# Optimization experiments

Hardware: AMD Instinct MI355X
Metric: run time of the kernel (lower is better)

The kernel has to match this reference:

```python
import jax, jax.numpy as jnp
import numpy as np

B, L, D = 1, 2048, 512
NL, N, K = 4, 16, 4
DI = 2 * D          # mamba expand=2
R = D // 16         # dt_rank = ceil(D/16)
H = 4 * D           # mlp hidden


def _ln(x, w, b, eps=1e-5):
    mu = x.mean(-1, keepdims=True)
    v = ((x - mu) ** 2).mean(-1, keepdims=True)
    return (x - mu) * jax.lax.rsqrt(v + eps) * w + b


def _rms(x, w, eps=1e-5):
    return x * jax.lax.rsqrt((x * x).mean(-1, keepdims=True) + eps) * w


def _ssm_scan(delta, Bm, Cm, u, A, Dp):
    # delta,u: (B,L,DI); Bm,Cm: (B,L,N); A: (DI,N); Dp: (DI,)
    def step(h, inp):
        d_t, b_t, c_t, u_t = inp                              # (B,DI),(B,N),(B,N),(B,DI)
        dA = jnp.exp(d_t[..., None] * A)                      # (B,DI,N)
        h = dA * h + (d_t * u_t)[..., None] * b_t[:, None, :]
        y = jnp.einsum('bdn,bn->bd', h, c_t)
        return h, y
    h0 = jnp.zeros((delta.shape[0], DI, N), delta.dtype)
    xs = (delta.swapaxes(0, 1), Bm.swapaxes(0, 1), Cm.swapaxes(0, 1), u.swapaxes(0, 1))
    _, ys = jax.lax.scan(step, h0, xs)
    return ys.swapaxes(0, 1) + u * Dp


def _mamba(h, in_w, cw, cb, xw, dtw, dtb, A_log, Dp, ow):
    xz = h @ in_w.T                                           # (B,L,2*DI)
    x, z = jnp.split(xz, 2, axis=-1)
    # causal depthwise conv1d, kernel K, left pad K-1
    xp = jnp.pad(x, ((0, 0), (K - 1, 0), (0, 0)))
    Ls = x.shape[1]
    x = sum(cw[:, k] * xp[:, k:k + Ls, :] for k in range(K)) + cb
    x = jax.nn.silu(x)
    dbc = x @ xw.T                                            # (B,L,R+2N)
    dt, Bm, Cm = dbc[..., :R], dbc[..., R:R + N], dbc[..., R + N:]
    delta = jax.nn.softplus(dt @ dtw.T + dtb)                 # (B,L,DI)
    A = -jnp.exp(A_log)                                       # (DI,N)
    y = _ssm_scan(delta, Bm, Cm, x, A, Dp)
    y = y * jax.nn.silu(z)
    return y @ ow.T


def _forward(hidden_states, ln1_w, ln1_b, in_proj_w, conv_w, conv_b, x_proj_w,
             dt_proj_w, dt_proj_b, A_log, D_param, out_proj_w, block_norm_w,
             norm_f_w, ln2_w, ln2_b, fc1_w, fc1_b, fc2_w, fc2_b):
    shortcut = hidden_states
    h = _ln(hidden_states, ln1_w, ln1_b)
    residual = None
    for i in range(in_proj_w.shape[0]):
        residual = h if residual is None else h + residual    # residual_in_fp32
        hn = _rms(residual, block_norm_w[i])                  # fused_add_norm prenorm
        h = _mamba(hn, in_proj_w[i], conv_w[i], conv_b[i], x_proj_w[i],
                   dt_proj_w[i], dt_proj_b[i], A_log[i], D_param[i], out_proj_w[i])
    h = _rms(h + residual, norm_f_w)                          # final rms_norm_fn
    h = shortcut + h
    x = _ln(h, ln2_w, ln2_b)
    x = jax.nn.gelu(x @ fc1_w.T + fc1_b)
    x = x @ fc2_w.T + fc2_b
    return h + x


def setup_inputs() -> dict:
    key = jax.random.key(0)
    ks = jax.random.split(key, 9)
    s = 0.02
    return {
        'hidden_states': jax.random.normal(ks[0], (B, L, D), jnp.float32),
        'ln1_w': jnp.ones((D,), jnp.float32),
        'ln1_b': jnp.zeros((D,), jnp.float32),
        'in_proj_w': jax.random.normal(ks[1], (NL, 2 * DI, D), jnp.float32) * s,
        'conv_w': jax.random.normal(ks[2], (NL, DI, K), jnp.float32) * 0.3,
        'conv_b': jnp.zeros((NL, DI), jnp.float32),
        'x_proj_w': jax.random.normal(ks[3], (NL, R + 2 * N, DI), jnp.float32) * s,
        'dt_proj_w': jax.random.normal(ks[4], (NL, DI, R), jnp.float32) * s,
        'dt_proj_b': jax.random.uniform(ks[5], (NL, DI), jnp.float32, -4.0, -2.0),
        'A_log': jnp.tile(jnp.log(jnp.arange(1, N + 1, dtype=jnp.float32)), (NL, DI, 1)),
        'D_param': jnp.ones((NL, DI), jnp.float32),
        'out_proj_w': jax.random.normal(ks[6], (NL, D, DI), jnp.float32) * s,
        'block_norm_w': jnp.ones((NL, D), jnp.float32),
        'norm_f_w': jnp.ones((D,), jnp.float32),
        'ln2_w': jnp.ones((D,), jnp.float32),
        'ln2_b': jnp.zeros((D,), jnp.float32),
        'fc1_w': jax.random.normal(ks[7], (H, D), jnp.float32) * s,
        'fc1_b': jnp.zeros((H,), jnp.float32),
        'fc2_w': jax.random.normal(ks[8], (D, H), jnp.float32) * s,
        'fc2_b': jnp.zeros((D,), jnp.float32),
    }


def reference(hidden_states, ln1_w, ln1_b, in_proj_w, conv_w, conv_b, x_proj_w,
              dt_proj_w, dt_proj_b, A_log, D_param, out_proj_w, block_norm_w,
              norm_f_w, ln2_w, ln2_b, fc1_w, fc1_b, fc2_w, fc2_b):
    return _forward(hidden_states, ln1_w, ln1_b, in_proj_w, conv_w, conv_b,
                    x_proj_w, dt_proj_w, dt_proj_b, A_log, D_param, out_proj_w,
                    block_norm_w, norm_f_w, ln2_w, ln2_b, fc1_w, fc1_b, fc2_w, fc2_b)
```

## Files before the change

kernel.cpp:

```cpp
#include <hip/hip_runtime.h>
#include <hip/hip_bf16.h>
#include <math.h>

#define L_SEQ 2048
#define Dm    512
#define DI    1024
#define Nst   16
#define Kc    4
#define Rr    32
#define NL    4
#define CH    128
#define LC    (L_SEQ / CH)

typedef __attribute__((ext_vector_type(8))) short bf16x8;
typedef __attribute__((ext_vector_type(4))) float f32x4;

__device__ __forceinline__ float act_softplus(float x) {
    return fmaxf(x, 0.f) + log1pf(__expf(-fabsf(x)));
}
__device__ __forceinline__ float act_gelu(float x) {
    float c = 0.7978845608028654f * (x + 0.044715f * x * x * x);
    float t = 1.f - 2.f / (__expf(2.f * c) + 1.f);
    return 0.5f * x * (1.f + t);
}
__device__ __forceinline__ float silu_(float x) {
    return x / (1.f + __expf(-x));
}
__device__ __forceinline__ ushort f2bf(float f) {
    union { float f; unsigned u; } c; c.f = f;
    unsigned r = c.u + 0x7fffu + ((c.u >> 16) & 1u);
    return (ushort)(r >> 16);
}
__device__ __forceinline__ float bf2f(ushort u) {
    union { unsigned u; float f; } c; c.u = ((unsigned)u) << 16;
    return c.f;
}
__device__ __forceinline__ float wave_sum(float v) {
    #pragma unroll
    for (int off = 32; off; off >>= 1) v += __shfl_xor(v, off);
    return v;
}

__global__ __launch_bounds__(256) void cast_all_kernel(
    const float* __restrict__ s0, ushort* __restrict__ d0, int n0,
    const float* __restrict__ s1, ushort* __restrict__ d1, int n1,
    const float* __restrict__ s2, ushort* __restrict__ d2, int n2,
    const float* __restrict__ s3, ushort* __restrict__ d3, int n3,
    const float* __restrict__ s4, ushort* __restrict__ d4, int n4_,
    const float* __restrict__ s5, ushort* __restrict__ d5, int n5)
{
    int i = blockIdx.x * 256 + threadIdx.x;
    const float* s; ushort* d;
    if (i < n0) { s = s0; d = d0; }
    else { i -= n0; if (i < n1) { s = s1; d = d1; }
    else { i -= n1; if (i < n2) { s = s2; d = d2; }
    else { i -= n2; if (i < n3) { s = s3; d = d3; }
    else { i -= n3; if (i < n4_) { s = s4; d = d4; }
    else { i -= n4_; if (i < n5) { s = s5; d = d5; } else return; } } } } }
    float4 v = ((const float4*)s)[i];
    ushort4 o;
    o.x = f2bf(v.x); o.y = f2bf(v.y); o.z = f2bf(v.z); o.w = f2bf(v.w);
    ((ushort4*)d)[i] = o;
}

__global__ __launch_bounds__(256) void ln_rms_kernel(const float* __restrict__ x,
    const float* __restrict__ w, const float* __restrict__ b,
    const float* __restrict__ rw, float* __restrict__ res,
    ushort* __restrict__ hn_bf)
{
    int lane = threadIdx.x & 63, wv = threadIdx.x >> 6;
    int row = blockIdx.x * 4 + wv;
    size_t base = (size_t)row * Dm + lane * 8;
    float v[8];
    *(float4*)(v)     = *(const float4*)(x + base);
    *(float4*)(v + 4) = *(const float4*)(x + base + 4);
    float s = 0.f, ss = 0.f;
    #pragma unroll
    for (int q = 0; q < 8; ++q) { s += v[q]; ss += v[q] * v[q]; }
    s = wave_sum(s); ss = wave_sum(ss);
    float mu = s * (1.f / Dm);
    float rs = rsqrtf(ss * (1.f / Dm) - mu * mu + 1e-5f);
    float wv8[8], bv8[8], rv8[8];
    *(float4*)(wv8)     = *(const float4*)(w + lane * 8);
    *(float4*)(wv8 + 4) = *(const float4*)(w + lane * 8 + 4);
    *(float4*)(bv8)     = *(const float4*)(b + lane * 8);
    *(float4*)(bv8 + 4) = *(const float4*)(b + lane * 8 + 4);
    *(float4*)(rv8)     = *(const float4*)(rw + lane * 8);
    *(float4*)(rv8 + 4) = *(const float4*)(rw + lane * 8 + 4);
    float o[8], ss2 = 0.f;
    #pragma unroll
    for (int q = 0; q < 8; ++q) {
        o[q] = (v[q] - mu) * rs * wv8[q] + bv8[q];
        ss2 += o[q] * o[q];
    }
    *(float4*)(res + base)     = *(float4*)(o);
    *(float4*)(res + base + 4) = *(float4*)(o + 4);
    ss2 = wave_sum(ss2);
    float rr = rsqrtf(ss2 * (1.f / Dm) + 1e-5f);
    bf16x8 hb;
    #pragma unroll
    for (int q = 0; q < 8; ++q) hb[q] = (short)f2bf(o[q] * rr * rv8[q]);
    *(bf16x8*)(hn_bf + base) = hb;
}

__global__ __launch_bounds__(256) void add_rms_kernel(const ushort* __restrict__ hb,
    float* __restrict__ res, const float* __restrict__ w, ushort* __restrict__ rms_out)
{
    int lane = threadIdx.x & 63, wv = threadIdx.x >> 6;
    int row = blockIdx.x * 4 + wv;
    size_t base = (size_t)row * Dm + lane * 8;
    bf16x8 hv = *(const bf16x8*)(hb + base);
    float v[8];
    *(float4*)(v)     = *(const float4*)(res + base);
    *(float4*)(v + 4) = *(const float4*)(res + base + 4);
    float ss = 0.f;
    #pragma unroll
    for (int q = 0; q < 8; ++q) {
        v[q] += bf2f((ushort)hv[q]);
        ss += v[q] * v[q];
    }
    *(float4*)(res + base)     = *(float4*)(v);
    *(float4*)(res + base + 4) = *(float4*)(v + 4);
    ss = wave_sum(ss);
    float rr = rsqrtf(ss * (1.f / Dm) + 1e-5f);
    float wv8[8];
    *(float4*)(wv8)     = *(const float4*)(w + lane * 8);
    *(float4*)(wv8 + 4) = *(const float4*)(w + lane * 8 + 4);
    bf16x8 ob;
    #pragma unroll
    for (int q = 0; q < 8; ++q) ob[q] = (short)f2bf(v[q] * rr * wv8[q]);
    *(bf16x8*)(rms_out + base) = ob;
}

__global__ __launch_bounds__(256) void final_ln2_kernel(const ushort* __restrict__ hb,
    const float* __restrict__ res, const float* __restrict__ shortcut,
    const float* __restrict__ wf, const float* __restrict__ w2,
    const float* __restrict__ b2, float* __restrict__ hout,
    ushort* __restrict__ yb16)
{
    int lane = threadIdx.x & 63, wv = threadIdx.x >> 6;
    int row = blockIdx.x * 4 + wv;
    size_t base = (size_t)row * Dm + lane * 8;
    bf16x8 hv = *(const bf16x8*)(hb + base);
    float v[8];
    *(float4*)(v)     = *(const float4*)(res + base);
    *(float4*)(v + 4) = *(const float4*)(res + base + 4);
    float ss = 0.f;
    #pragma unroll
    for (int q = 0; q < 8; ++q) {
        v[q] += bf2f((ushort)hv[q]);
        ss += v[q] * v[q];
    }
    ss = wave_sum(ss);
    float rs = rsqrtf(ss * (1.f / Dm) + 1e-5f);
    float sc[8], wf8[8];
    *(float4*)(sc)     = *(const float4*)(shortcut + base);
    *(float4*)(sc + 4) = *(const float4*)(shortcut + base + 4);
    *(float4*)(wf8)     = *(const float4*)(wf + lane * 8);
    *(float4*)(wf8 + 4) = *(const float4*)(wf + lane * 8 + 4);
    float t[8], s2 = 0.f, ss2 = 0.f;
    #pragma unroll
    for (int q = 0; q < 8; ++q) {
        t[q] = sc[q] + v[q] * rs * wf8[q];
        s2 += t[q]; ss2 += t[q] * t[q];
    }
    *(float4*)(hout + base)     = *(float4*)(t);
    *(float4*)(hout + base + 4) = *(float4*)(t + 4);
    s2 = wave_sum(s2); ss2 = wave_sum(ss2);
    float mu = s2 * (1.f / Dm);
    float rsig = rsqrtf(ss2 * (1.f / Dm) - mu * mu + 1e-5f);
    float w28[8], b28[8];
    *(float4*)(w28)     = *(const float4*)(w2 + lane * 8);
    *(float4*)(w28 + 4) = *(const float4*)(w2 + lane * 8 + 4);
    *(float4*)(b28)     = *(const float4*)(b2 + lane * 8);
    *(float4*)(b28 + 4) = *(const float4*)(b2 + lane * 8 + 4);
    bf16x8 ob;
    #pragma unroll
    for (int q = 0; q < 8; ++q) ob[q] = (short)f2bf((t[q] - mu) * rsig * w28[q] + b28[q]);
    *(bf16x8*)(yb16 + base) = ob;
}

template<int BM, int BN, int BK, int EPI, int KS = 1>
__global__ __launch_bounds__(256) void gemm_mfma(
    const ushort* __restrict__ A, int lda,
    const ushort* __restrict__ W, int K,
    void* __restrict__ Cout, int ldc,
    const float* __restrict__ bias, const float* __restrict__ addsrc,
    size_t split_stride)
{
    constexpr int ROWB  = BK * 2;
    constexpr int SMASK = (ROWB / 16) - 1;
    constexpr int KK    = BK / 32;
    constexpr int WM = BM / 2, WN = BN / 2;
    constexpr int FM = WM / 16, FN = WN / 16;
    constexpr int ISS_A = (BM * ROWB) / 4096;
    constexpr int ISS_W = (BN * ROWB) / 4096;

    __shared__ __align__(16) ushort As[BM * BK];
    __shared__ __align__(16) ushort Ws[BN * BK];

    int tid = threadIdx.x;
    int wave = tid >> 6, lane = tid & 63;
    int wr = wave >> 1, wc = wave & 1;
    int l16 = lane & 15, lk = lane >> 4;
    int bm = blockIdx.y * BM, bn = blockIdx.x * BN;

    int kbeg = 0, kend = K;
    float* coutf = (float*)Cout;
    if constexpr (KS > 1) {
        int Kper = K / KS;
        kbeg = blockIdx.z * Kper; kend = kbeg + Kper;
        coutf += split_stride * blockIdx.z;
    }

    const ushort* srcA[ISS_A];
    const ushort* srcW[ISS_W];
    #pragma unroll
    for (int s = 0; s < ISS_A; ++s) {
        int off = s * 4096 + wave * 1024 + lane * 16;
        int row = off / ROWB;
        int slot = (off % ROWB) >> 4;
        int col = ((slot ^ (row & SMASK)) << 3);
        srcA[s] = A + (size_t)(bm + row) * lda + col;
    }
    #pragma unroll
    for (int s = 0; s < ISS_W; ++s) {
        int off = s * 4096 + wave * 1024 + lane * 16;
        int row = off / ROWB;
        int slot = (off % ROWB) >> 4;
        int col = ((slot ^ (row & SMASK)) << 3);
        srcW[s] = W + (size_t)(bn + row) * K + col;
    }
    int aoff[FM][KK], woff[FN][KK];
    #pragma unroll
    for (int i = 0; i < FM; ++i) {
        int row = wr * WM + i * 16 + l16;
        #pragma unroll
        for (int kk = 0; kk < KK; ++kk)
            aoff[i][kk] = row * BK + ((((kk << 2) | lk) ^ (row & SMASK)) << 3);
    }
    #pragma unroll
    for (int j = 0; j < FN; ++j) {
        int row = wc * WN + j * 16 + l16;
        #pragma unroll
        for (int kk = 0; kk < KK; ++kk)
            woff[j][kk] = row * BK + ((((kk << 2) | lk) ^ (row & SMASK)) << 3);
    }

    f32x4 acc[FM][FN] = {};

    for (int k0 = kbeg; k0 < kend; k0 += BK) {
        #pragma unroll
        for (int s = 0; s < ISS_A; ++s)
            __builtin_amdgcn_global_load_lds(
                (const __attribute__((address_space(1))) void*)(srcA[s] + k0),
                (__attribute__((address_space(3))) void*)((char*)As + s * 4096 + wave * 1024),
                16, 0, 0);
        #pragma unroll
        for (int s = 0; s < ISS_W; ++s)
            __builtin_amdgcn_global_load_lds(
                (const __attribute__((address_space(1))) void*)(srcW[s] + k0),
                (__attribute__((address_space(3))) void*)((char*)Ws + s * 4096 + wave * 1024),
                16, 0, 0);
        __syncthreads();
        #pragma unroll
        for (int kk = 0; kk < KK; ++kk) {
            bf16x8 af[FM], wf[FN];
            #pragma unroll
            for (int i = 0; i < FM; ++i) af[i] = *(const bf16x8*)(As + aoff[i][kk]);
            #pragma unroll
            for (int j = 0; j < FN; ++j) wf[j] = *(const bf16x8*)(Ws + woff[j][kk]);
            #pragma unroll
            for (int i = 0; i < FM; ++i)
                #pragma unroll
                for (int j = 0; j < FN; ++j)
                    acc[i][j] = __builtin_amdgcn_mfma_f32_16x16x32_bf16(af[i], wf[j], acc[i][j], 0, 0, 0);
        }
        __syncthreads();
    }

    int orow0 = bm + wr * WM, ocol0 = bn + wc * WN;
    #pragma unroll
    for (int j = 0; j < FN; ++j) {
        int col = ocol0 + j * 16 + l16;
        float bj = 0.f;
        if constexpr (EPI == 2 || EPI == 4) bj = bias[col];
        #pragma unroll
        for (int i = 0; i < FM; ++i) {
            #pragma unroll
            for (int r = 0; r < 4; ++r) {
                int row = orow0 + i * 16 + lk * 4 + r;
                float v = acc[i][j][r];
                if constexpr (EPI == 0) {
                    coutf[(size_t)row * ldc + col] = v;
                } else if constexpr (EPI == 1) {
                    ((ushort*)Cout)[(size_t)row * ldc + col] = f2bf(v);
                } else if constexpr (EPI == 2) {
                    ((ushort*)Cout)[(size_t)row * ldc + col] = f2bf(act_gelu(v + bj));
                } else if constexpr (EPI == 4) {
                    ((float*)Cout)[(size_t)row * ldc + col] = v + bj + addsrc[(size_t)row * ldc + col];
                }
            }
        }
    }
}

__global__ __launch_bounds__(256) void xfin_kernel(
    const float* __restrict__ part, const ushort* __restrict__ wdt,
    const float* __restrict__ dtb, float* __restrict__ dbc,
    ushort* __restrict__ delta_bf)
{
    __shared__ float sdt[8][32];
    int tid = threadIdx.x;
    int t0 = blockIdx.x * 8;
    const int S = L_SEQ * 64;
    #pragma unroll
    for (int i = tid; i < 512; i += 256) {
        int tt = i >> 6, c = i & 63;
        int idx = (t0 + tt) * 64 + c;
        float s = part[idx] + part[idx + S] + part[idx + 2 * S] + part[idx + 3 * S];
        if (c < 32) sdt[tt][c] = s;
        else dbc[idx] = s;
    }
    __syncthreads();
    int d0 = tid * 4;
    bf16x8 w[4][4];
    float b4[4];
    #pragma unroll
    for (int q = 0; q < 4; ++q) {
        b4[q] = dtb[d0 + q];
        #pragma unroll
        for (int p = 0; p < 4; ++p)
            w[q][p] = *(const bf16x8*)(wdt + (size_t)(d0 + q) * 32 + p * 8);
    }
    for (int tt = 0; tt < 8; ++tt) {
        float acc[4] = { b4[0], b4[1], b4[2], b4[3] };
        #pragma unroll
        for (int p = 0; p < 4; ++p)
            #pragma unroll
            for (int e = 0; e < 8; ++e) {
                float sv = sdt[tt][p * 8 + e];
                #pragma unroll
                for (int q = 0; q < 4; ++q)
                    acc[q] = fmaf(sv, bf2f((ushort)w[q][p][e]), acc[q]);
            }
        ushort4 o;
        o.x = f2bf(act_softplus(acc[0]));
        o.y = f2bf(act_softplus(acc[1]));
        o.z = f2bf(act_softplus(acc[2]));
        o.w = f2bf(act_softplus(acc[3]));
        *(ushort4*)(delta_bf + (size_t)(t0 + tt) * DI + d0) = o;
    }
}

__global__ __launch_bounds__(256) void conv_silu_kernel(const ushort* __restrict__ xz,
    const float* __restrict__ cw, const float* __restrict__ cb, ushort* __restrict__ xc)
{
    int g = blockIdx.x * 256 + threadIdx.x;
    int e = g * 8;
    int d0 = e & (DI - 1);
    int t = e >> 10;
    float acc[8];
    #pragma unroll
    for (int q = 0; q < 8; ++q) acc[q] = cb[d0 + q];
    float4 cwv[8];
    #pragma unroll
    for (int q = 0; q < 8; ++q) cwv[q] = *(const float4*)(cw + (size_t)(d0 + q) * 4);
    #pragma unroll
    for (int k = 0; k < 4; ++k) {
        int tt = t + k - 3;
        if (tt >= 0) {
            bf16x8 xv = *(const bf16x8*)(xz + (size_t)tt * (2 * DI) + d0);
            #pragma unroll
            for (int q = 0; q < 8; ++q) {
                float wk = (k == 0) ? cwv[q].x : (k == 1) ? cwv[q].y : (k == 2) ? cwv[q].z : cwv[q].w;
                acc[q] = fmaf(wk, bf2f((ushort)xv[q]), acc[q]);
            }
        }
    }
    bf16x8 o;
    #pragma unroll
    for (int q = 0; q < 8; ++q) o[q] = (short)f2bf(silu_(acc[q]));
    *(bf16x8*)(xc + e) = o;
}

__global__ __launch_bounds__(256) void scan_chunk_kernel(
    const ushort* __restrict__ delta, const ushort* __restrict__ u,
    const float* __restrict__ dbc, const float* __restrict__ A_log,
    float* __restrict__ hend, float* __restrict__ aprod)
{
    __shared__ float bs[LC][16];
    int tid = threadIdx.x;
    int c = blockIdx.x;
    int d = blockIdx.y * 256 + tid;
    int t0 = c * LC;
    {
        int tt = tid >> 4, nn = tid & 15;
        bs[tt][nn] = dbc[(size_t)(t0 + tt) * 64 + 32 + nn];
    }
    float A2[16];
    {
        float a[16];
        #pragma unroll
        for (int q = 0; q < 4; ++q)
            *(float4*)(a + q * 4) = ((const float4*)(A_log + (size_t)d * 16))[q];
        #pragma unroll
        for (int n = 0; n < 16; ++n)
            A2[n] = -__expf(a[n]) * 1.44269504f;
    }
    float h[16], ap[16];
    #pragma unroll
    for (int n = 0; n < 16; ++n) { h[n] = 0.f; ap[n] = 1.f; }
    __syncthreads();
    for (int tt = 0; tt < LC; ++tt) {
        int t = t0 + tt;
        float dt_ = bf2f(delta[(size_t)t * DI + d]);
        float du = dt_ * bf2f(u[(size_t)t * DI + d]);
        #pragma unroll
        for (int n = 0; n < 16; ++n) {
            float dA = exp2f(dt_ * A2[n]);
            h[n] = fmaf(dA, h[n], du * bs[tt][n]);
            ap[n] *= dA;
        }
    }
    size_t base = ((size_t)c * DI + d) * 16;
    #pragma unroll
    for (int q = 0; q < 4; ++q) {
        ((float4*)(hend + base))[q]  = *(float4*)(h + q * 4);
        ((float4*)(aprod + base))[q] = *(float4*)(ap + q * 4);
    }
}

__global__ __launch_bounds__(64) void chunk_prefix_kernel(
    const float* __restrict__ hend, float* __restrict__ aprod_hin)
{
    int j = blockIdx.x * 64 + threadIdx.x;
    float h = 0.f;
    for (int cg = 0; cg < CH; cg += 8) {
        float ap[8], he[8];
        #pragma unroll
        for (int q = 0; q < 8; ++q) {
            size_t o = (size_t)(cg + q) * (DI * Nst) + j;
            ap[q] = aprod_hin[o]; he[q] = hend[o];
        }
        #pragma unroll
        for (int q = 0; q < 8; ++q) {
            size_t o = (size_t)(cg + q) * (DI * Nst) + j;
            aprod_hin[o] = h;
            h = fmaf(ap[q], h, he[q]);
        }
    }
}

__global__ __launch_bounds__(256) void scan_apply_kernel(
    const ushort* __restrict__ delta, const ushort* __restrict__ u,
    const float* __restrict__ dbc, const float* __restrict__ A_log,
    const float* __restrict__ Dp, const ushort* __restrict__ xz,
    const float* __restrict__ hin, ushort* __restrict__ y)
{
    __shared__ float bs[LC][16], cs[LC][16];
    int tid = threadIdx.x;
    int c = blockIdx.x;
    int d = blockIdx.y * 256 + tid;
    int t0 = c * LC;
    #pragma unroll
    for (int i = tid; i < LC * 32; i += 256) {
        int tt = i >> 5, k = i & 31;
        float v = dbc[(size_t)(t0 + tt) * 64 + 32 + k];
        if (k < 16) bs[tt][k] = v; else cs[tt][k - 16] = v;
    }
    float A2[16];
    {
        float a[16];
        #pragma unroll
        for (int q = 0; q < 4; ++q)
            *(float4*)(a + q * 4) = ((const float4*)(A_log + (size_t)d * 16))[q];
        #pragma unroll
        for (int n = 0; n < 16; ++n)
            A2[n] = -__expf(a[n]) * 1.44269504f;
    }
    float h[16];
    size_t base = ((size_t)c * DI + d) * 16;
    #pragma unroll
    for (int q = 0; q < 4; ++q)
        *(float4*)(h + q * 4) = ((const float4*)(hin + base))[q];
    float Dval = Dp[d];
    __syncthreads();
    for (int tt = 0; tt < LC; ++tt) {
        int t = t0 + tt;
        float dt_ = bf2f(delta[(size_t)t * DI + d]);
        float u_  = bf2f(u[(size_t)t * DI + d]);
        float du  = dt_ * u_;
        float acc = 0.f;
        #pragma unroll
        for (int n = 0; n < 16; ++n) {
            float dA = exp2f(dt_ * A2[n]);
            h[n] = fmaf(dA, h[n], du * bs[tt][n]);
            acc = fmaf(h[n], cs[tt][n], acc);
        }
        float z = bf2f(xz[(size_t)t * (2 * DI) + DI + d]);
        y[(size_t)t * DI + d] = f2bf((acc + u_ * Dval) * silu_(z));
    }
}

extern "C" void kernel_launch(void* const* d_in, const int* in_sizes, int n_in,
                              void* d_out, int out_size, void* d_ws, size_t ws_size,
                              hipStream_t stream)
{
    const float* hidden     = (const float*)d_in[0];
    const float* ln1_w      = (const float*)d_in[1];
    const float* ln1_b      = (const float*)d_in[2];
    const float* in_proj_w  = (const float*)d_in[3];
    const float* conv_w     = (const float*)d_in[4];
    const float* conv_b     = (const float*)d_in[5];
    const float* x_proj_w   = (const float*)d_in[6];
    const float* dt_proj_w  = (const float*)d_in[7];
    const float* dt_proj_b  = (const float*)d_in[8];
    const float* A_log      = (const float*)d_in[9];
    const float* D_param    = (const float*)d_in[10];
    const float* out_proj_w = (const float*)d_in[11];
    const float* block_norm_w = (const float*)d_in[12];
    const float* norm_f_w   = (const float*)d_in[13];
    const float* ln2_w      = (const float*)d_in[14];
    const float* ln2_b      = (const float*)d_in[15];
    const float* fc1_w      = (const float*)d_in[16];
    const float* fc1_b      = (const float*)d_in[17];
    const float* fc2_w      = (const float*)d_in[18];
    const float* fc2_b      = (const float*)d_in[19];

    char* P = (char*)d_ws;
    auto alloc = [&](size_t bytes) { char* r = P; P += (bytes + 255) & ~(size_t)255; return r; };
    float* hout   = (float*)alloc((size_t)L_SEQ * Dm * 4);
    float* res    = (float*)alloc((size_t)L_SEQ * Dm * 4);
    float* dbc    = (float*)alloc((size_t)L_SEQ * 64 * 4);
    float* part   = (float*)alloc((size_t)4 * L_SEQ * 64 * 4);
    float* hend   = (float*)alloc((size_t)CH * DI * Nst * 4);
    float* aprod  = (float*)alloc((size_t)CH * DI * Nst * 4);
    ushort* h_bf  = (ushort*)alloc((size_t)L_SEQ * Dm * 2);
    ushort* delta_bf = (ushort*)alloc((size_t)L_SEQ * DI * 2);
    ushort* hn_bf = (ushort*)alloc((size_t)L_SEQ * Dm * 2);
    ushort* xz_bf = (ushort*)alloc((size_t)L_SEQ * 2 * DI * 2);
    ushort* xc_bf = (ushort*)alloc((size_t)L_SEQ * DI * 2);
    ushort* yb_bf = (ushort*)alloc((size_t)L_SEQ * DI * 2);
    ushort* w_in  = (ushort*)alloc((size_t)NL * 2 * DI * Dm * 2);
    ushort* w_out = (ushort*)alloc((size_t)NL * Dm * DI * 2);
    ushort* w_x   = (ushort*)alloc((size_t)NL * 64 * DI * 2);
    ushort* w_dt  = (ushort*)alloc((size_t)NL * DI * Rr * 2);
    ushort* w_fc1 = (ushort*)alloc((size_t)(4 * Dm) * Dm * 2);
    ushort* w_fc2 = (ushort*)alloc((size_t)Dm * (4 * Dm) * 2);
    float* out  = (float*)d_out;

    {
        int n0 = NL * 2 * DI * Dm / 4, n1 = NL * Dm * DI / 4, n2 = NL * 64 * DI / 4;
        int n3 = NL * DI * Rr / 4, n4_ = 4 * Dm * Dm / 4, n5 = Dm * 4 * Dm / 4;
        int tot = n0 + n1 + n2 + n3 + n4_ + n5;
        cast_all_kernel<<<(tot + 255) / 256, 256, 0, stream>>>(
            in_proj_w, w_in, n0, out_proj_w, w_out, n1, x_proj_w, w_x, n2,
            dt_proj_w, w_dt, n3, fc1_w, w_fc1, n4_, fc2_w, w_fc2, n5);
    }

    ln_rms_kernel<<<L_SEQ / 4, 256, 0, stream>>>(hidden, ln1_w, ln1_b,
                                                 block_norm_w, res, hn_bf);

    dim3 gscan(CH, DI / 256);
    for (int i = 0; i < NL; ++i) {
        if (i) add_rms_kernel<<<L_SEQ / 4, 256, 0, stream>>>(h_bf, res,
                                                  block_norm_w + i * Dm, hn_bf);
        gemm_mfma<128, 128, 128, 1><<<dim3(2 * DI / 128, L_SEQ / 128), 256, 0, stream>>>(
            hn_bf, Dm, w_in + (size_t)i * 2 * DI * Dm, Dm, xz_bf, 2 * DI, nullptr, nullptr, 0);
        conv_silu_kernel<<<(L_SEQ * DI / 8) / 256, 256, 0, stream>>>(
            xz_bf, conv_w + i * DI * Kc, conv_b + i * DI, xc_bf);
        gemm_mfma<64, 64, 64, 0, 4><<<dim3(1, L_SEQ / 64, 4), 256, 0, stream>>>(
            xc_bf, DI, w_x + (size_t)i * 64 * DI, DI, part, 64, nullptr, nullptr,
            (size_t)L_SEQ * 64);
        xfin_kernel<<<L_SEQ / 8, 256, 0, stream>>>(part, w_dt + (size_t)i * DI * Rr,
                                        dt_proj_b + i * DI, dbc, delta_bf);
        scan_chunk_kernel<<<gscan, 256, 0, stream>>>(delta_bf, xc_bf, dbc,
                                        A_log + (size_t)i * DI * Nst, hend, aprod);
        chunk_prefix_kernel<<<(DI * Nst) / 64, 64, 0, stream>>>(hend, aprod);
        scan_apply_kernel<<<gscan, 256, 0, stream>>>(delta_bf, xc_bf, dbc,
                                        A_log + (size_t)i * DI * Nst,
                                        D_param + i * DI, xz_bf, aprod, yb_bf);
        gemm_mfma<64, 64, 128, 1><<<dim3(Dm / 64, L_SEQ / 64), 256, 0, stream>>>(
            yb_bf, DI, w_out + (size_t)i * Dm * DI, DI, h_bf, Dm, nullptr, nullptr, 0);
    }

    final_ln2_kernel<<<L_SEQ / 4, 256, 0, stream>>>(h_bf, res, hidden, norm_f_w,
                                                ln2_w, ln2_b, hout, hn_bf);
    gemm_mfma<128, 128, 128, 2><<<dim3(2048 / 128, L_SEQ / 128), 256, 0, stream>>>(
        hn_bf, Dm, w_fc1, Dm, xz_bf, 2048, fc1_b, nullptr, 0);
    gemm_mfma<64, 64, 128, 4><<<dim3(Dm / 64, L_SEQ / 64), 256, 0, stream>>>(
        xz_bf, 2048, w_fc2, 2048, out, Dm, fc2_b, hout, 0);
}
```

Baseline: 445.4 us.

## Fuse conv+silu into x_proj GEMM and dt_proj+softplus into scan kernels

The causal conv and SiLU are now computed inside the split-K x_proj GEMM prologue, which writes xc and stages the A tile in LDS directly. The xfin kernel and the delta buffer are removed. Split-K partials are reduced and dt_proj plus softplus are recomputed per timestep inside both scan kernels. Each layer drops two launches and the delta/dbc round-trips, at the cost of recomputing the 32-term dt projection twice per element and re-reducing the partials in every scan block.

```diff
diff --git a/kernel.cpp b/kernel.cpp
--- a/kernel.cpp
+++ b/kernel.cpp
@@ -180,13 +180,12 @@
     *(bf16x8*)(yb16 + base) = ob;
 }
 
-template<int BM, int BN, int BK, int EPI, int KS = 1>
+template<int BM, int BN, int BK, int EPI>
 __global__ __launch_bounds__(256) void gemm_mfma(
     const ushort* __restrict__ A, int lda,
     const ushort* __restrict__ W, int K,
     void* __restrict__ Cout, int ldc,
-    const float* __restrict__ bias, const float* __restrict__ addsrc,
-    size_t split_stride)
+    const float* __restrict__ bias, const float* __restrict__ addsrc)
 {
     constexpr int ROWB  = BK * 2;
     constexpr int SMASK = (ROWB / 16) - 1;
@@ -205,14 +204,6 @@
     int l16 = lane & 15, lk = lane >> 4;
     int bm = blockIdx.y * BM, bn = blockIdx.x * BN;
 
-    int kbeg = 0, kend = K;
-    float* coutf = (float*)Cout;
-    if constexpr (KS > 1) {
-        int Kper = K / KS;
-        kbeg = blockIdx.z * Kper; kend = kbeg + Kper;
-        coutf += split_stride * blockIdx.z;
-    }
-
     const ushort* srcA[ISS_A];
     const ushort* srcW[ISS_W];
     #pragma unroll
@@ -249,7 +240,7 @@
 
     f32x4 acc[FM][FN] = {};
 
-    for (int k0 = kbeg; k0 < kend; k0 += BK) {
+    for (int k0 = 0; k0 < K; k0 += BK) {
         #pragma unroll
         for (int s = 0; s < ISS_A; ++s)
             __builtin_amdgcn_global_load_lds(
@@ -291,9 +282,7 @@
             for (int r = 0; r < 4; ++r) {
                 int row = orow0 + i * 16 + lk * 4 + r;
                 float v = acc[i][j][r];
-                if constexpr (EPI == 0) {
-                    coutf[(size_t)row * ldc + col] = v;
-                } else if constexpr (EPI == 1) {
+                if constexpr (EPI == 1) {
                     ((ushort*)Cout)[(size_t)row * ldc + col] = f2bf(v);
                 } else if constexpr (EPI == 2) {
                     ((ushort*)Cout)[(size_t)row * ldc + col] = f2bf(act_gelu(v + bj));
@@ -305,99 +294,150 @@
     }
 }
 
-__global__ __launch_bounds__(256) void xfin_kernel(
-    const float* __restrict__ part, const ushort* __restrict__ wdt,
-    const float* __restrict__ dtb, float* __restrict__ dbc,
-    ushort* __restrict__ delta_bf)
-{
-    __shared__ float sdt[8][32];
+__global__ __launch_bounds__(256) void xproj_conv_kernel(
+    const ushort* __restrict__ xz, const float* __restrict__ cw,
+    const float* __restrict__ cb, const ushort* __restrict__ W,
+    ushort* __restrict__ xc, float* __restrict__ part)
+{
+    constexpr int BM = 64, BN = 64, BK = 64;
+    constexpr int ROWB  = BK * 2;
+    constexpr int SMASK = (ROWB / 16) - 1;
+    constexpr int KK    = BK / 32;
+    constexpr int WM = 32, WN = 32, FM = 2, FN = 2;
+
+    __shared__ __align__(16) ushort As[BM * BK];
+    __shared__ __align__(16) ushort Ws[BN * BK];
+
     int tid = threadIdx.x;
-    int t0 = blockIdx.x * 8;
-    const int S = L_SEQ * 64;
-    #pragma unroll
-    for (int i = tid; i < 512; i += 256) {
-        int tt = i >> 6, c = i & 63;
-        int idx = (t0 + tt) * 64 + c;
-        float s = part[idx] + part[idx + S] + part[idx + 2 * S] + part[idx + 3 * S];
-        if (c < 32) sdt[tt][c] = s;
-        else dbc[idx] = s;
-    }
-    __syncthreads();
-    int d0 = tid * 4;
-    bf16x8 w[4][4];
-    float b4[4];
-    #pragma unroll
-    for (int q = 0; q < 4; ++q) {
-        b4[q] = dtb[d0 + q];
-        #pragma unroll
-        for (int p = 0; p < 4; ++p)
-            w[q][p] = *(const bf16x8*)(wdt + (size_t)(d0 + q) * 32 + p * 8);
-    }
-    for (int tt = 0; tt < 8; ++tt) {
-        float acc[4] = { b4[0], b4[1], b4[2], b4[3] };
-        #pragma unroll
-        for (int p = 0; p < 4; ++p)
-            #pragma unroll
-            for (int e = 0; e < 8; ++e) {
-                float sv = sdt[tt][p * 8 + e];
+    int wave = tid >> 6, lane = tid & 63;
+    int wr = wave >> 1, wc = wave & 1;
+    int l16 = lane & 15, lk = lane >> 4;
+    int bm = blockIdx.y * BM;
+    int z = blockIdx.z;
+    int kbeg = z * (DI / 4);
+
+    const ushort* srcW[2];
+    #pragma unroll
+    for (int s = 0; s < 2; ++s) {
+        int off = s * 4096 + wave * 1024 + lane * 16;
+        int row = off / ROWB;
+        int slot = (off % ROWB) >> 4;
+        int col = ((slot ^ (row & SMASK)) << 3);
+        srcW[s] = W + (size_t)row * DI + kbeg + col;
+    }
+    int aoff[FM][KK], woff[FN][KK];
+    #pragma unroll
+    for (int i = 0; i < FM; ++i) {
+        int row = wr * WM + i * 16 + l16;
+        #pragma unroll
+        for (int kk = 0; kk < KK; ++kk)
+            aoff[i][kk] = row * BK + ((((kk << 2) | lk) ^ (row & SMASK)) << 3);
+    }
+    #pragma unroll
+    for (int j = 0; j < FN; ++j) {
+        int row = wc * WN + j * 16 + l16;
+        #pragma unroll
+        for (int kk = 0; kk < KK; ++kk)
+            woff[j][kk] = row * BK + ((((kk << 2) | lk) ^ (row & SMASK)) << 3);
+    }
+
+    f32x4 acc[FM][FN] = {};
+
+    for (int k0 = 0; k0 < DI / 4; k0 += BK) {
+        #pragma unroll
+        for (int s = 0; s < 2; ++s)
+            __builtin_amdgcn_global_load_lds(
+                (const __attribute__((address_space(1))) void*)(srcW[s] + k0),
+                (__attribute__((address_space(3))) void*)((char*)Ws + s * 4096 + wave * 1024),
+                16, 0, 0);
+        #pragma unroll
+        for (int s = 0; s < 2; ++s) {
+            int off = s * 4096 + wave * 1024 + lane * 16;
+            int row = off >> 7;
+            int slot = (off >> 4) & 7;
+            int t = bm + row;
+            int dcol = kbeg + k0 + slot * 8;
+            float a[8];
+            float4 c4[8];
+            #pragma unroll
+            for (int q = 0; q < 8; ++q) {
+                a[q] = cb[dcol + q];
+                c4[q] = *(const float4*)(cw + (size_t)(dcol + q) * 4);
+            }
+            #pragma unroll
+            for (int k = 0; k < 4; ++k) {
+                int tt = t + k - 3;
+                if (tt >= 0) {
+                    bf16x8 xv = *(const bf16x8*)(xz + (size_t)tt * (2 * DI) + dcol);
+                    #pragma unroll
+                    for (int q = 0; q < 8; ++q) {
+                        float wk = (k == 0) ? c4[q].x : (k == 1) ? c4[q].y
+                                 : (k == 2) ? c4[q].z : c4[q].w;
+                        a[q] = fmaf(wk, bf2f((ushort)xv[q]), a[q]);
+                    }
+                }
+            }
+            bf16x8 o;
+            #pragma unroll
+            for (int q = 0; q < 8; ++q) o[q] = (short)f2bf(silu_(a[q]));
+            *(bf16x8*)(xc + (size_t)t * DI + dcol) = o;
+            *(bf16x8*)(As + row * BK + ((slot ^ (row & SMASK)) << 3)) = o;
+        }
+        __syncthreads();
+        #pragma unroll
+        for (int kk = 0; kk < KK; ++kk) {
+            bf16x8 af[FM], wf[FN];
+            #pragma unroll
+            for (int i = 0; i < FM; ++i) af[i] = *(const bf16x8*)(As + aoff[i][kk]);
+            #pragma unroll
+            for (int j = 0; j < FN; ++j) wf[j] = *(const bf16x8*)(Ws + woff[j][kk]);
+            #pragma unroll
+            for (int i = 0; i < FM; ++i)
                 #pragma unroll
-                for (int q = 0; q < 4; ++q)
-                    acc[q] = fmaf(sv, bf2f((ushort)w[q][p][e]), acc[q]);
+                for (int j = 0; j < FN; ++j)
+                    acc[i][j] = __builtin_amdgcn_mfma_f32_16x16x32_bf16(af[i], wf[j], acc[i][j], 0, 0, 0);
+        }
+        __syncthreads();
+    }
+
+    float* coutf = part + (size_t)z * L_SEQ * 64;
+    int orow0 = bm + wr * WM, ocol0 = wc * WN;
+    #pragma unroll
+    for (int j = 0; j < FN; ++j) {
+        int col = ocol0 + j * 16 + l16;
+        #pragma unroll
+        for (int i = 0; i < FM; ++i)
+            #pragma unroll
+            for (int r = 0; r < 4; ++r) {
+                int row = orow0 + i * 16 + lk * 4 + r;
+                coutf[(size_t)row * 64 + col] = acc[i][j][r];
             }
-        ushort4 o;
-        o.x = f2bf(act_softplus(acc[0]));
-        o.y = f2bf(act_softplus(acc[1]));
-        o.z = f2bf(act_softplus(acc[2]));
-        o.w = f2bf(act_softplus(acc[3]));
-        *(ushort4*)(delta_bf + (size_t)(t0 + tt) * DI + d0) = o;
-    }
-}
-
-__global__ __launch_bounds__(256) void conv_silu_kernel(const ushort* __restrict__ xz,
-    const float* __restrict__ cw, const float* __restrict__ cb, ushort* __restrict__ xc)
-{
-    int g = blockIdx.x * 256 + threadIdx.x;
-    int e = g * 8;
-    int d0 = e & (DI - 1);
-    int t = e >> 10;
-    float acc[8];
-    #pragma unroll
-    for (int q = 0; q < 8; ++q) acc[q] = cb[d0 + q];
-    float4 cwv[8];
-    #pragma unroll
-    for (int q = 0; q < 8; ++q) cwv[q] = *(const float4*)(cw + (size_t)(d0 + q) * 4);
-    #pragma unroll
-    for (int k = 0; k < 4; ++k) {
-        int tt = t + k - 3;
-        if (tt >= 0) {
-            bf16x8 xv = *(const bf16x8*)(xz + (size_t)tt * (2 * DI) + d0);
-            #pragma unroll
-            for (int q = 0; q < 8; ++q) {
-                float wk = (k == 0) ? cwv[q].x : (k == 1) ? cwv[q].y : (k == 2) ? cwv[q].z : cwv[q].w;
-                acc[q] = fmaf(wk, bf2f((ushort)xv[q]), acc[q]);
-            }
-        }
-    }
-    bf16x8 o;
-    #pragma unroll
-    for (int q = 0; q < 8; ++q) o[q] = (short)f2bf(silu_(acc[q]));
-    *(bf16x8*)(xc + e) = o;
+    }
 }
 
 __global__ __launch_bounds__(256) void scan_chunk_kernel(
-    const ushort* __restrict__ delta, const ushort* __restrict__ u,
-    const float* __restrict__ dbc, const float* __restrict__ A_log,
+    const float* __restrict__ part, const ushort* __restrict__ u,
+    const ushort* __restrict__ wdt, const float* __restrict__ dtb,
+    const float* __restrict__ A_log,
     float* __restrict__ hend, float* __restrict__ aprod)
 {
-    __shared__ float bs[LC][16];
+    __shared__ float sdt[LC][32];
+    __shared__ float bsm[LC][16];
     int tid = threadIdx.x;
     int c = blockIdx.x;
     int d = blockIdx.y * 256 + tid;
     int t0 = c * LC;
-    {
-        int tt = tid >> 4, nn = tid & 15;
-        bs[tt][nn] = dbc[(size_t)(t0 + tt) * 64 + 32 + nn];
-    }
+    const int S = L_SEQ * 64;
+    for (int i = tid; i < LC * 48; i += 256) {
+        int tt = i / 48, cc = i % 48;
+        int idx = (t0 + tt) * 64 + cc;
+        float s = part[idx] + part[idx + S] + part[idx + 2 * S] + part[idx + 3 * S];
+        if (cc < 32) sdt[tt][cc] = s; else bsm[tt][cc - 32] = s;
+    }
+    bf16x8 wd[4];
+    #pragma unroll
+    for (int p = 0; p < 4; ++p) wd[p] = *(const bf16x8*)(wdt + (size_t)d * 32 + p * 8);
+    float bd = dtb[d];
     float A2[16];
     {
         float a[16];
@@ -414,12 +454,18 @@
     __syncthreads();
     for (int tt = 0; tt < LC; ++tt) {
         int t = t0 + tt;
-        float dt_ = bf2f(delta[(size_t)t * DI + d]);
-        float du = dt_ * bf2f(u[(size_t)t * DI + d]);
+        float dtv = bd;
+        #pragma unroll
+        for (int p = 0; p < 4; ++p)
+            #pragma unroll
+            for (int e = 0; e < 8; ++e)
+                dtv = fmaf(sdt[tt][p * 8 + e], bf2f((ushort)wd[p][e]), dtv);
+        dtv = act_softplus(dtv);
+        float du = dtv * bf2f(u[(size_t)t * DI + d]);
         #pragma unroll
         for (int n = 0; n < 16; ++n) {
-            float dA = exp2f(dt_ * A2[n]);
-            h[n] = fmaf(dA, h[n], du * bs[tt][n]);
+            float dA = exp2f(dtv * A2[n]);
+            h[n] = fmaf(dA, h[n], du * bsm[tt][n]);
             ap[n] *= dA;
         }
     }
@@ -453,22 +499,31 @@
 }
 
 __global__ __launch_bounds__(256) void scan_apply_kernel(
-    const ushort* __restrict__ delta, const ushort* __restrict__ u,
-    const float* __restrict__ dbc, const float* __restrict__ A_log,
-    const float* __restrict__ Dp, const ushort* __restrict__ xz,
-    const float* __restrict__ hin, ushort* __restrict__ y)
-{
-    __shared__ float bs[LC][16], cs[LC][16];
+    const float* __restrict__ part, const ushort* __restrict__ u,
+    const ushort* __restrict__ wdt, const float* __restrict__ dtb,
+    const float* __restrict__ A_log, const float* __restrict__ Dp,
+    const ushort* __restrict__ xz, const float* __restrict__ hin,
+    ushort* __restrict__ y)
+{
+    __shared__ float sdt[LC][32];
+    __shared__ float bsm[LC][16], csm[LC][16];
     int tid = threadIdx.x;
     int c = blockIdx.x;
     int d = blockIdx.y * 256 + tid;
     int t0 = c * LC;
-    #pragma unroll
-    for (int i = tid; i < LC * 32; i += 256) {
-        int tt = i >> 5, k = i & 31;
-        float v = dbc[(size_t)(t0 + tt) * 64 + 32 + k];
-        if (k < 16) bs[tt][k] = v; else cs[tt][k - 16] = v;
-    }
+    const int S = L_SEQ * 64;
+    for (int i = tid; i < LC * 64; i += 256) {
+        int tt = i >> 6, cc = i & 63;
+        int idx = (t0 + tt) * 64 + cc;
+        float s = part[idx] + part[idx + S] + part[idx + 2 * S] + part[idx + 3 * S];
+        if (cc < 32) sdt[tt][cc] = s;
+        else if (cc < 48) bsm[tt][cc - 32] = s;
+        else csm[tt][cc - 48] = s;
+    }
+    bf16x8 wd[4];
+    #pragma unroll
+    for (int p = 0; p < 4; ++p) wd[p] = *(const bf16x8*)(wdt + (size_t)d * 32 + p * 8);
+    float bd = dtb[d];
     float A2[16];
     {
         float a[16];
@@ -488,18 +543,24 @@
     __syncthreads();
     for (int tt = 0; tt < LC; ++tt) {
         int t = t0 + tt;
-        float dt_ = bf2f(delta[(size_t)t * DI + d]);
-        float u_  = bf2f(u[(size_t)t * DI + d]);
-        float du  = dt_ * u_;
+        float dtv = bd;
+        #pragma unroll
+        for (int p = 0; p < 4; ++p)
+            #pragma unroll
+            for (int e = 0; e < 8; ++e)
+                dtv = fmaf(sdt[tt][p * 8 + e], bf2f((ushort)wd[p][e]), dtv);
+        dtv = act_softplus(dtv);
+        float u_ = bf2f(u[(size_t)t * DI + d]);
+        float du = dtv * u_;
         float acc = 0.f;
         #pragma unroll
         for (int n = 0; n < 16; ++n) {
-            float dA = exp2f(dt_ * A2[n]);
-            h[n] = fmaf(dA, h[n], du * bs[tt][n]);
-            acc = fmaf(h[n], cs[tt][n], acc);
-        }
-        float z = bf2f(xz[(size_t)t * (2 * DI) + DI + d]);
-        y[(size_t)t * DI + d] = f2bf((acc + u_ * Dval) * silu_(z));
+            float dA = exp2f(dtv * A2[n]);
+            h[n] = fmaf(dA, h[n], du * bsm[tt][n]);
+            acc = fmaf(h[n], csm[tt][n], acc);
+        }
+        float zv = bf2f(xz[(size_t)t * (2 * DI) + DI + d]);
+        y[(size_t)t * DI + d] = f2bf((acc + u_ * Dval) * silu_(zv));
     }
 }
 
@@ -532,12 +593,10 @@
     auto alloc = [&](size_t bytes) { char* r = P; P += (bytes + 255) & ~(size_t)255; return r; };
     float* hout   = (float*)alloc((size_t)L_SEQ * Dm * 4);
     float* res    = (float*)alloc((size_t)L_SEQ * Dm * 4);
-    float* dbc    = (float*)alloc((size_t)L_SEQ * 64 * 4);
     float* part   = (float*)alloc((size_t)4 * L_SEQ * 64 * 4);
     float* hend   = (float*)alloc((size_t)CH * DI * Nst * 4);
     float* aprod  = (float*)alloc((size_t)CH * DI * Nst * 4);
     ushort* h_bf  = (ushort*)alloc((size_t)L_SEQ * Dm * 2);
-    ushort* delta_bf = (ushort*)alloc((size_t)L_SEQ * DI * 2);
     ushort* hn_bf = (ushort*)alloc((size_t)L_SEQ * Dm * 2);
     ushort* xz_bf = (ushort*)alloc((size_t)L_SEQ * 2 * DI * 2);
     ushort* xc_bf = (ushort*)alloc((size_t)L_SEQ * DI * 2);
@@ -567,28 +626,26 @@
         if (i) add_rms_kernel<<<L_SEQ / 4, 256, 0, stream>>>(h_bf, res,
                                                   block_norm_w + i * Dm, hn_bf);
         gemm_mfma<128, 128, 128, 1><<<dim3(2 * DI / 128, L_SEQ / 128), 256, 0, stream>>>(
-            hn_bf, Dm, w_in + (size_t)i * 2 * DI * Dm, Dm, xz_bf, 2 * DI, nullptr, nullptr, 0);
-        conv_silu_kernel<<<(L_SEQ * DI / 8) / 256, 256, 0, stream>>>(
-            xz_bf, conv_w + i * DI * Kc, conv_b + i * DI, xc_bf);
-        gemm_mfma<64, 64, 64, 0, 4><<<dim3(1, L_SEQ / 64, 4), 256, 0, stream>>>(
-            xc_bf, DI, w_x + (size_t)i * 64 * DI, DI, part, 64, nullptr, nullptr,
-            (size_t)L_SEQ * 64);
-        xfin_kernel<<<L_SEQ / 8, 256, 0, stream>>>(part, w_dt + (size_t)i * DI * Rr,
-                                        dt_proj_b + i * DI, dbc, delta_bf);
-        scan_chunk_kernel<<<gscan, 256, 0, stream>>>(delta_bf, xc_bf, dbc,
+            hn_bf, Dm, w_in + (size_t)i * 2 * DI * Dm, Dm, xz_bf, 2 * DI, nullptr, nullptr);
+        xproj_conv_kernel<<<dim3(1, L_SEQ / 64, 4), 256, 0, stream>>>(
+            xz_bf, conv_w + i * DI * Kc, conv_b + i * DI,
+            w_x + (size_t)i * 64 * DI, xc_bf, part);
+        scan_chunk_kernel<<<gscan, 256, 0, stream>>>(part, xc_bf,
+                                        w_dt + (size_t)i * DI * Rr, dt_proj_b + i * DI,
                                         A_log + (size_t)i * DI * Nst, hend, aprod);
         chunk_prefix_kernel<<<(DI * Nst) / 64, 64, 0, stream>>>(hend, aprod);
-        scan_apply_kernel<<<gscan, 256, 0, stream>>>(delta_bf, xc_bf, dbc,
+        scan_apply_kernel<<<gscan, 256, 0, stream>>>(part, xc_bf,
+                                        w_dt + (size_t)i * DI * Rr, dt_proj_b + i * DI,
                                         A_log + (size_t)i * DI * Nst,
                                         D_param + i * DI, xz_bf, aprod, yb_bf);
         gemm_mfma<64, 64, 128, 1><<<dim3(Dm / 64, L_SEQ / 64), 256, 0, stream>>>(
-            yb_bf, DI, w_out + (size_t)i * Dm * DI, DI, h_bf, Dm, nullptr, nullptr, 0);
+            yb_bf, DI, w_out + (size_t)i * Dm * DI, DI, h_bf, Dm, nullptr, nullptr);
     }
 
     final_ln2_kernel<<<L_SEQ / 4, 256, 0, stream>>>(h_bf, res, hidden, norm_f_w,
                                                 ln2_w, ln2_b, hout, hn_bf);
     gemm_mfma<128, 128, 128, 2><<<dim3(2048 / 128, L_SEQ / 128), 256, 0, stream>>>(
-        hn_bf, Dm, w_fc1, Dm, xz_bf, 2048, fc1_b, nullptr, 0);
+        hn_bf, Dm, w_fc1, Dm, xz_bf, 2048, fc1_b, nullptr);
     gemm_mfma<64, 64, 128, 4><<<dim3(Dm / 64, L_SEQ / 64), 256, 0, stream>>>(
-        xz_bf, 2048, w_fc2, 2048, out, Dm, fc2_b, hout, 0);
-}
+        xz_bf, 2048, w_fc2, 2048, out, Dm, fc2_b, hout);
+}
```

New measurement: 476.7 us. +7.0%, slower.

## Fuse split-K reduction and dt projection into the chunked scan kernel

Applied to the files above, without the earlier changes.

Removes the separate xfin kernel. The split-K partial sums of x_proj are now reduced inside scan_chunk and scan_apply, and the dt_proj matvec plus softplus is computed per channel inside scan_chunk, which also writes delta for the apply pass. The x_proj split-K factor rises from 4 to 8 for more parallelism in that skinny GEMM. This drops one launch and the dbc buffer per layer, at the cost of reducing partials redundantly in every scan block and doing 32 FMAs per timestep serially in the scan loop.

```diff
diff --git a/kernel.cpp b/kernel.cpp
--- a/kernel.cpp
+++ b/kernel.cpp
@@ -11,6 +11,7 @@
 #define NL    4
 #define CH    128
 #define LC    (L_SEQ / CH)
+#define KSX   8
 
 typedef __attribute__((ext_vector_type(8))) short bf16x8;
 typedef __attribute__((ext_vector_type(4))) float f32x4;
@@ -305,54 +306,6 @@
     }
 }
 
-__global__ __launch_bounds__(256) void xfin_kernel(
-    const float* __restrict__ part, const ushort* __restrict__ wdt,
-    const float* __restrict__ dtb, float* __restrict__ dbc,
-    ushort* __restrict__ delta_bf)
-{
-    __shared__ float sdt[8][32];
-    int tid = threadIdx.x;
-    int t0 = blockIdx.x * 8;
-    const int S = L_SEQ * 64;
-    #pragma unroll
-    for (int i = tid; i < 512; i += 256) {
-        int tt = i >> 6, c = i & 63;
-        int idx = (t0 + tt) * 64 + c;
-        float s = part[idx] + part[idx + S] + part[idx + 2 * S] + part[idx + 3 * S];
-        if (c < 32) sdt[tt][c] = s;
-        else dbc[idx] = s;
-    }
-    __syncthreads();
-    int d0 = tid * 4;
-    bf16x8 w[4][4];
-    float b4[4];
-    #pragma unroll
-    for (int q = 0; q < 4; ++q) {
-        b4[q] = dtb[d0 + q];
-        #pragma unroll
-        for (int p = 0; p < 4; ++p)
-            w[q][p] = *(const bf16x8*)(wdt + (size_t)(d0 + q) * 32 + p * 8);
-    }
-    for (int tt = 0; tt < 8; ++tt) {
-        float acc[4] = { b4[0], b4[1], b4[2], b4[3] };
-        #pragma unroll
-        for (int p = 0; p < 4; ++p)
-            #pragma unroll
-            for (int e = 0; e < 8; ++e) {
-                float sv = sdt[tt][p * 8 + e];
-                #pragma unroll
-                for (int q = 0; q < 4; ++q)
-                    acc[q] = fmaf(sv, bf2f((ushort)w[q][p][e]), acc[q]);
-            }
-        ushort4 o;
-        o.x = f2bf(act_softplus(acc[0]));
-        o.y = f2bf(act_softplus(acc[1]));
-        o.z = f2bf(act_softplus(acc[2]));
-        o.w = f2bf(act_softplus(acc[3]));
-        *(ushort4*)(delta_bf + (size_t)(t0 + tt) * DI + d0) = o;
-    }
-}
-
 __global__ __launch_bounds__(256) void conv_silu_kernel(const ushort* __restrict__ xz,
     const float* __restrict__ cw, const float* __restrict__ cb, ushort* __restrict__ xc)
 {
@@ -385,19 +338,31 @@
 }
 
 __global__ __launch_bounds__(256) void scan_chunk_kernel(
-    const ushort* __restrict__ delta, const ushort* __restrict__ u,
-    const float* __restrict__ dbc, const float* __restrict__ A_log,
-    float* __restrict__ hend, float* __restrict__ aprod)
-{
-    __shared__ float bs[LC][16];
+    const float* __restrict__ part, const ushort* __restrict__ u,
+    const ushort* __restrict__ wdt, const float* __restrict__ dtb,
+    const float* __restrict__ A_log,
+    float* __restrict__ hend, float* __restrict__ aprod,
+    ushort* __restrict__ delta_bf)
+{
+    __shared__ float sdt[LC][32];
+    __shared__ float bsm[LC][16];
     int tid = threadIdx.x;
     int c = blockIdx.x;
     int d = blockIdx.y * 256 + tid;
     int t0 = c * LC;
-    {
-        int tt = tid >> 4, nn = tid & 15;
-        bs[tt][nn] = dbc[(size_t)(t0 + tt) * 64 + 32 + nn];
-    }
+    const int S = L_SEQ * 64;
+    for (int i = tid; i < LC * 48; i += 256) {
+        int tt = i / 48, cc = i % 48;
+        int idx = (t0 + tt) * 64 + cc;
+        float s = 0.f;
+        #pragma unroll
+        for (int p = 0; p < KSX; ++p) s += part[idx + p * S];
+        if (cc < 32) sdt[tt][cc] = s; else bsm[tt][cc - 32] = s;
+    }
+    bf16x8 wd[4];
+    #pragma unroll
+    for (int p = 0; p < 4; ++p) wd[p] = *(const bf16x8*)(wdt + (size_t)d * 32 + p * 8);
+    float bd = dtb[d];
     float A2[16];
     {
         float a[16];
@@ -414,12 +379,20 @@
     __syncthreads();
     for (int tt = 0; tt < LC; ++tt) {
         int t = t0 + tt;
-        float dt_ = bf2f(delta[(size_t)t * DI + d]);
+        float dtv = bd;
+        #pragma unroll
+        for (int p = 0; p < 4; ++p)
+            #pragma unroll
+            for (int e = 0; e < 8; ++e)
+                dtv = fmaf(sdt[tt][p * 8 + e], bf2f((ushort)wd[p][e]), dtv);
+        ushort dbf = f2bf(act_softplus(dtv));
+        delta_bf[(size_t)t * DI + d] = dbf;
+        float dt_ = bf2f(dbf);
         float du = dt_ * bf2f(u[(size_t)t * DI + d]);
         #pragma unroll
         for (int n = 0; n < 16; ++n) {
             float dA = exp2f(dt_ * A2[n]);
-            h[n] = fmaf(dA, h[n], du * bs[tt][n]);
+            h[n] = fmaf(dA, h[n], du * bsm[tt][n]);
             ap[n] *= dA;
         }
     }
@@ -453,21 +426,24 @@
 }
 
 __global__ __launch_bounds__(256) void scan_apply_kernel(
-    const ushort* __restrict__ delta, const ushort* __restrict__ u,
-    const float* __restrict__ dbc, const float* __restrict__ A_log,
+    const float* __restrict__ part, const ushort* __restrict__ delta,
+    const ushort* __restrict__ u, const float* __restrict__ A_log,
     const float* __restrict__ Dp, const ushort* __restrict__ xz,
     const float* __restrict__ hin, ushort* __restrict__ y)
 {
-    __shared__ float bs[LC][16], cs[LC][16];
+    __shared__ float bsm[LC][16], csm[LC][16];
     int tid = threadIdx.x;
     int c = blockIdx.x;
     int d = blockIdx.y * 256 + tid;
     int t0 = c * LC;
-    #pragma unroll
+    const int S = L_SEQ * 64;
     for (int i = tid; i < LC * 32; i += 256) {
         int tt = i >> 5, k = i & 31;
-        float v = dbc[(size_t)(t0 + tt) * 64 + 32 + k];
-        if (k < 16) bs[tt][k] = v; else cs[tt][k - 16] = v;
+        int idx = (t0 + tt) * 64 + 32 + k;
+        float s = 0.f;
+        #pragma unroll
+        for (int p = 0; p < KSX; ++p) s += part[idx + p * S];
+        if (k < 16) bsm[tt][k] = s; else csm[tt][k - 16] = s;
     }
     float A2[16];
     {
@@ -495,11 +471,11 @@
         #pragma unroll
         for (int n = 0; n < 16; ++n) {
             float dA = exp2f(dt_ * A2[n]);
-            h[n] = fmaf(dA, h[n], du * bs[tt][n]);
-            acc = fmaf(h[n], cs[tt][n], acc);
-        }
-        float z = bf2f(xz[(size_t)t * (2 * DI) + DI + d]);
-        y[(size_t)t * DI + d] = f2bf((acc + u_ * Dval) * silu_(z));
+            h[n] = fmaf(dA, h[n], du * bsm[tt][n]);
+            acc = fmaf(h[n], csm[tt][n], acc);
+        }
+        float zv = bf2f(xz[(size_t)t * (2 * DI) + DI + d]);
+        y[(size_t)t * DI + d] = f2bf((acc + u_ * Dval) * silu_(zv));
     }
 }
 
@@ -532,8 +508,7 @@
     auto alloc = [&](size_t bytes) { char* r = P; P += (bytes + 255) & ~(size_t)255; return r; };
     float* hout   = (float*)alloc((size_t)L_SEQ * Dm * 4);
     float* res    = (float*)alloc((size_t)L_SEQ * Dm * 4);
-    float* dbc    = (float*)alloc((size_t)L_SEQ * 64 * 4);
-    float* part   = (float*)alloc((size_t)4 * L_SEQ * 64 * 4);
+    float* part   = (float*)alloc((size_t)KSX * L_SEQ * 64 * 4);
     float* hend   = (float*)alloc((size_t)CH * DI * Nst * 4);
     float* aprod  = (float*)alloc((size_t)CH * DI * Nst * 4);
     ushort* h_bf  = (ushort*)alloc((size_t)L_SEQ * Dm * 2);
@@ -570,15 +545,14 @@
             hn_bf, Dm, w_in + (size_t)i * 2 * DI * Dm, Dm, xz_bf, 2 * DI, nullptr, nullptr, 0);
         conv_silu_kernel<<<(L_SEQ * DI / 8) / 256, 256, 0, stream>>>(
             xz_bf, conv_w + i * DI * Kc, conv_b + i * DI, xc_bf);
-        gemm_mfma<64, 64, 64, 0, 4><<<dim3(1, L_SEQ / 64, 4), 256, 0, stream>>>(
+        gemm_mfma<64, 64, 64, 0, KSX><<<dim3(1, L_SEQ / 64, KSX), 256, 0, stream>>>(
             xc_bf, DI, w_x + (size_t)i * 64 * DI, DI, part, 64, nullptr, nullptr,
             (size_t)L_SEQ * 64);
-        xfin_kernel<<<L_SEQ / 8, 256, 0, stream>>>(part, w_dt + (size_t)i * DI * Rr,
-                                        dt_proj_b + i * DI, dbc, delta_bf);
-        scan_chunk_kernel<<<gscan, 256, 0, stream>>>(delta_bf, xc_bf, dbc,
-                                        A_log + (size_t)i * DI * Nst, hend, aprod);
+        scan_chunk_kernel<<<gscan, 256, 0, stream>>>(part, xc_bf,
+                                        w_dt + (size_t)i * DI * Rr, dt_proj_b + i * DI,
+                                        A_log + (size_t)i * DI * Nst, hend, aprod, delta_bf);
         chunk_prefix_kernel<<<(DI * Nst) / 64, 64, 0, stream>>>(hend, aprod);
-        scan_apply_kernel<<<gscan, 256, 0, stream>>>(delta_bf, xc_bf, dbc,
+        scan_apply_kernel<<<gscan, 256, 0, stream>>>(part, delta_bf, xc_bf,
                                         A_log + (size_t)i * DI * Nst,
                                         D_param + i * DI, xz_bf, aprod, yb_bf);
         gemm_mfma<64, 64, 128, 1><<<dim3(Dm / 64, L_SEQ / 64), 256, 0, stream>>>(
```

Measured after the change: 429.5 us. 3.6% less time.
